# Optimization experiments

Measured on AMD Instinct MI355X. Metric: run time of the kernel, lower is better.

## Reference

```python
import jax, jax.numpy as jnp
import numpy as np
from jax import lax

NEG = -1e30  # log-space -inf surrogate

def setup_inputs() -> dict:
    key = jax.random.key(0)
    ks = jax.random.split(key, 6)
    B, T, D, V, Lmax = 16, 800, 512, 4000, 100
    hs_pad = jax.random.normal(ks[0], (B, T, D), dtype=jnp.float32)
    W = jax.random.normal(ks[1], (D, V), dtype=jnp.float32) * 0.02
    b = jnp.zeros((V,), dtype=jnp.float32)
    hlens = jax.random.randint(ks[2], (B,), 400, T + 1, dtype=jnp.int32)
    ys_pad = jax.random.randint(ks[3], (B, Lmax), 1, V, dtype=jnp.int32)
    ys_lens = jax.random.randint(ks[4], (B,), 50, Lmax + 1, dtype=jnp.int32)
    return {"hs_pad": hs_pad, "W": W, "b": b, "hlens": hlens,
            "ys_pad": ys_pad, "ys_lens": ys_lens}

def _ctc_loss(lp, ys_pad, hlens, ys_lens):
    # lp: [T, B, V] log-probs; blank = 0
    T, B, V = lp.shape
    Lmax = ys_pad.shape[1]
    S = 2 * Lmax + 1  # extended label length: blank-interleaved
    ext = jnp.zeros((B, S), dtype=ys_pad.dtype).at[:, 1::2].set(ys_pad)
    # skip transition s-2 -> s allowed when ext[s] != blank and ext[s] != ext[s-2]
    skip = jnp.concatenate(
        [jnp.zeros((B, 2), dtype=bool),
         (ext[:, 2:] != 0) & (ext[:, 2:] != ext[:, :-2])], axis=1)
    # per-frame emission log-probs for extended labels: [T, B, S]
    emit = jnp.take_along_axis(lp, jnp.broadcast_to(ext[None], (T, B, S)), axis=2)
    alpha0 = jnp.full((B, S), NEG, dtype=lp.dtype).at[:, :2].set(emit[0, :, :2])

    def step(alpha, inp):
        emit_t, active = inp  # [B, S], [B]
        s1 = jnp.pad(alpha[:, :-1], ((0, 0), (1, 0)), constant_values=NEG)
        s2 = jnp.pad(alpha[:, :-2], ((0, 0), (2, 0)), constant_values=NEG)
        s2 = jnp.where(skip, s2, NEG)
        new = jnp.logaddexp(jnp.logaddexp(alpha, s1), s2) + emit_t
        alpha = jnp.where(active[:, None], new, alpha)  # freeze past hlen
        return alpha, None

    active = jnp.arange(1, T)[:, None] < hlens[None, :]  # [T-1, B]
    alpha, _ = lax.scan(step, alpha0, (emit[1:], active))
    idx = (2 * ys_lens).astype(jnp.int32)  # last blank position
    a_last = jnp.take_along_axis(alpha, idx[:, None], axis=1)[:, 0]
    a_prev = jnp.take_along_axis(alpha, (idx - 1)[:, None], axis=1)[:, 0]
    loss = -jnp.logaddexp(a_last, a_prev)
    # zero_infinity=True
    return jnp.where(jnp.isfinite(loss) & (loss < 1e29), loss, 0.0)

def reference(hs_pad, W, b, hlens, ys_pad, ys_lens):
    # ctc_lo projection (dropout_rate=0.0) -> [T, B, V] -> log_softmax
    logits = jnp.einsum('btd,dv->btv', hs_pad, W) + b
    lp = jax.nn.log_softmax(logits, axis=-1).transpose(1, 0, 2)
    loss = _ctc_loss(lp, ys_pad, hlens, ys_lens)
    B = hs_pad.shape[0]
    return loss.sum() / B  # reduce=True: sum / batch size
```

## Files before the change

kernel.cpp:

```cpp
#include <hip/hip_runtime.h>
#include <hip/hip_bf16.h>
#include <math.h>

#define NEGV -1e30f
#define LN2F 0.6931471805599453f


typedef __attribute__((ext_vector_type(8))) short bf16x8;
typedef __attribute__((ext_vector_type(4))) float f32x4;

__device__ __forceinline__ short f2bf(float x) {
    __hip_bfloat16 h = __float2bfloat16(x);
    return __builtin_bit_cast(short, h);
}

__device__ __forceinline__ float shup1(float x) {
    return __builtin_bit_cast(float,
        __builtin_amdgcn_update_dpp(0, __builtin_bit_cast(int, x),
                                    0x138, 0xf, 0xf, true));
}

#define GLD_LDS(g, l) \
    __builtin_amdgcn_global_load_lds( \
        (const __attribute__((address_space(1))) void*)(g), \
        (__attribute__((address_space(3))) void*)(l), 16, 0, 0)

#define WAITV(n) do { \
    asm volatile("s_waitcnt vmcnt(" #n ")" ::: "memory"); \
    __builtin_amdgcn_sched_barrier(0); \
} while (0)

__global__ __launch_bounds__(256) void prep(
    const float* __restrict__ hs, const float* __restrict__ W,
    const float* __restrict__ bias, const int* __restrict__ ys,
    short* __restrict__ W2, short* __restrict__ A2,
    float* __restrict__ biasp, unsigned char* __restrict__ M,
    unsigned char* __restrict__ canon, float* __restrict__ lse_sum,
    float* __restrict__ out)
{
    __shared__ float tile[32][65];
    __shared__ unsigned char mapl[4096];
    const int bx = blockIdx.x, tid = threadIdx.x;

    if (bx < 1024) {
        const int n0 = (bx & 63) * 64;
        const int k0 = (bx >> 6) * 32;
        #pragma unroll
        for (int p = 0; p < 8; p++) {
            int idx = p * 256 + tid;
            int k = idx >> 6, n = idx & 63;
            int gn = n0 + n;
            tile[k][n] = (gn < 4000) ? W[(size_t)(k0 + k) * 4000 + gn] : 0.0f;
        }
        __syncthreads();
        const int nn = tid >> 6, lane = tid & 63;
        const int l16 = lane & 15, quad = lane >> 4;
        const int ct = n0 >> 7, wn = (n0 >> 6) & 1, it = k0 >> 5;
        size_t chunk = ((((size_t)ct * 16 + it) * 2 + wn) * 4 + nn) * 64 + lane;
        bf16x8 r;
        #pragma unroll
        for (int j = 0; j < 8; j++) r[j] = f2bf(tile[quad * 8 + j][nn * 16 + l16]);
        *(bf16x8*)(W2 + chunk * 8) = r;
    } else if (bx < 4224) {
        int g = (bx - 1024) * 256 + tid;
        int lane = g & 63, mi = (g >> 6) & 3, wm = (g >> 8) & 1;
        int it = (g >> 9) & 15, rb = g >> 13;
        int row = rb * 128 + wm * 64 + mi * 16 + (lane & 15);
        int k = it * 32 + (lane >> 4) * 8;
        const float* src = hs + (size_t)row * 512 + k;
        float4 u = *(const float4*)src;
        float4 v = *(const float4*)(src + 4);
        bf16x8 r;
        r[0] = f2bf(u.x); r[1] = f2bf(u.y); r[2] = f2bf(u.z); r[3] = f2bf(u.w);
        r[4] = f2bf(v.x); r[5] = f2bf(v.y); r[6] = f2bf(v.z); r[7] = f2bf(v.w);
        *(bf16x8*)(A2 + (size_t)g * 8) = r;
    } else if (bx < 4240) {
        const int b = bx - 4224;
        for (int i = tid; i < 1024; i += 256)
            ((unsigned int*)mapl)[i] = 0xFFFFFFFFu;
        __syncthreads();
        if (tid == 0) mapl[0] = 0;
        __syncthreads();
        if (tid < 100) mapl[ys[b * 100 + tid]] = (unsigned char)(tid + 1);
        __syncthreads();
        for (int i = tid; i < 1024; i += 256)
            ((unsigned int*)(M + (size_t)b * 4096))[i] = ((const unsigned int*)mapl)[i];
        if (tid < 128) {
            int colc = (tid >= 1 && tid <= 100) ? ys[b * 100 + tid - 1] : 0;
            canon[b * 128 + tid] = mapl[colc];
        }
    } else {
        for (int i = tid; i < 4096; i += 256)
            biasp[i] = (i < 4000) ? bias[i] : NEGV;
        for (int i = tid; i < 12800; i += 256)
            lse_sum[i] = 0.0f;
        if (tid == 0) out[0] = 0.0f;
    }
}

__global__ __launch_bounds__(512, 4) void lse_mfma(
    const short* __restrict__ A2,
    const short* __restrict__ W2,
    const float* __restrict__ biasp,
    const unsigned char* __restrict__ M,
    float* __restrict__ lse_sum,
    __hip_bfloat16* __restrict__ Praw)
{
    const unsigned int bid = blockIdx.x;
    const unsigned int xcd = bid & 7;
    const unsigned int s = bid >> 3;
    const unsigned int cp = s / 13;
    const unsigned int rl = s - cp * 13;
    const unsigned int rb = rl * 8 + xcd;
    if (rb >= 100) return;

    const int tid = threadIdx.x;
    const int w = tid >> 6, lane = tid & 63;
    const int quad = lane >> 4, l16 = lane & 15;
    const int wm = w >> 2;
    const int wc = w & 3;
    const int row0 = rb * 128;
    const int col0 = cp * 256;

    __shared__ __align__(16) short sbuf[3][12288];

    const short* gb[3];
    int lo[3];
    #pragma unroll
    for (int j = 0; j < 3; j++) {
        int sg = 3 * w + j;
        const short* cbase =
            (sg < 8)  ? (A2 + (size_t)rb * 65536)
          : (sg < 16) ? (W2 + (size_t)(2 * cp) * 65536)
                      : (W2 + (size_t)(2 * cp + 1) * 65536);
        gb[j] = cbase + (sg & 7) * 512 + lane * 8;
        lo[j] = sg * 512 + lane * 8;
    }

#define STAGE(s_, bi_) do { \
    GLD_LDS(gb[0] + (size_t)(s_) * 4096, &sbuf[bi_][lo[0]]); \
    GLD_LDS(gb[1] + (size_t)(s_) * 4096, &sbuf[bi_][lo[1]]); \
    GLD_LDS(gb[2] + (size_t)(s_) * 4096, &sbuf[bi_][lo[2]]); \
} while (0)

    f32x4 acc[4][4];
    #pragma unroll
    for (int mi = 0; mi < 4; mi++)
        #pragma unroll
        for (int ni = 0; ni < 4; ni++) acc[mi][ni] = (f32x4){0.f,0.f,0.f,0.f};

    STAGE(0, 0);
    STAGE(1, 1);
    WAITV(3);
    __builtin_amdgcn_s_barrier();
    __builtin_amdgcn_sched_barrier(0);

    const int boff = 4096 + (wc >> 1) * 4096 + (wc & 1) * 2048;

    #pragma unroll
    for (int it = 0; it < 16; ++it) {
        if (it + 2 < 16) STAGE(it + 2, (it + 2) % 3);

        const short* cb = &sbuf[it % 3][0];
        const short* ap = cb + wm * 2048 + lane * 8;
        const short* bp = cb + boff + lane * 8;
        bf16x8 af[4], bfr[4];
        #pragma unroll
        for (int mi = 0; mi < 4; mi++) af[mi]  = *(const bf16x8*)(ap + mi * 512);
        #pragma unroll
        for (int ni = 0; ni < 4; ni++) bfr[ni] = *(const bf16x8*)(bp + ni * 512);

        __builtin_amdgcn_s_setprio(1);
        #pragma unroll
        for (int mi = 0; mi < 4; mi++)
            #pragma unroll
            for (int ni = 0; ni < 4; ni++)
                acc[mi][ni] = __builtin_amdgcn_mfma_f32_16x16x32_bf16(
                    af[mi], bfr[ni], acc[mi][ni], 0, 0, 0);
        __builtin_amdgcn_s_setprio(0);

        if (it < 15) {
            if (it < 14) { WAITV(3); }
            else         { WAITV(0); }
            __builtin_amdgcn_s_barrier();
            __builtin_amdgcn_sched_barrier(0);
        }
    }
#undef STAGE
    __builtin_amdgcn_sched_barrier(0);

    const int b0i = row0 / 800;
    const int b1i = (b0i + 1 < 16) ? b0i + 1 : 15;
    const int bbound = (b0i + 1) * 800;
    float sv[16];
    #pragma unroll
    for (int i = 0; i < 16; i++) sv[i] = 0.0f;
    #pragma unroll
    for (int ni = 0; ni < 4; ni++) {
        int col = col0 + wc * 64 + ni * 16 + l16;
        float bj = biasp[col];
        unsigned char sl0 = M[(size_t)b0i * 4096 + col];
        unsigned char sl1 = M[(size_t)b1i * 4096 + col];
        #pragma unroll
        for (int mi = 0; mi < 4; mi++) {
            #pragma unroll
            for (int r = 0; r < 4; r++) {
                int row = row0 + wm * 64 + mi * 16 + quad * 4 + r;
                float v = acc[mi][ni][r] + bj;
                sv[mi * 4 + r] += __expf(v);
                unsigned char sl = (row < bbound) ? sl0 : sl1;
                if (sl != 255)
                    Praw[(size_t)row * 128 + sl] = __float2bfloat16(v);
            }
        }
    }
    #pragma unroll
    for (int off = 1; off < 16; off <<= 1)
        #pragma unroll
        for (int i = 0; i < 16; i++) sv[i] += __shfl_xor(sv[i], off);
    if (l16 == 0) {
        #pragma unroll
        for (int mi = 0; mi < 4; mi++)
            #pragma unroll
            for (int r = 0; r < 4; r++)
                atomicAdd(&lse_sum[row0 + wm * 64 + mi * 16 + quad * 4 + r],
                          sv[mi * 4 + r]);
    }
}

__global__ __launch_bounds__(256) void pexp(
    const __hip_bfloat16* __restrict__ Praw,
    const float* __restrict__ lse_sum,
    const unsigned char* __restrict__ canon,
    float* __restrict__ PE)
{
    __shared__ unsigned char st[224];
    __shared__ float scs[16];
    const int bp = blockIdx.x;
    const int b = bp / 50, rr = bp - b * 50;
    const int tid = threadIdx.x;
    const unsigned char* cb = canon + b * 128;
    if (tid < 224) {
        int idx = (tid + 1) >> 1;
        st[tid] = (tid & 1) ? cb[idx < 128 ? idx : 127] : (unsigned char)0;
    }
    const int row0 = b * 800 + rr * 16;
    if (tid < 16) scs[tid] = __builtin_amdgcn_rcpf(lse_sum[row0 + tid]) * 2048.0f;
    __syncthreads();
    for (int item = tid; item < 832; item += 256) {
        int i = item / 52, sg = item - i * 52;
        int row = row0 + i;
        const __hip_bfloat16* pr = Praw + (size_t)row * 128;
        float sc = scs[i];
        int s0 = sg * 4;
        float4 o;
        o.x = (s0 + 0 <= 200) ? __expf(__bfloat162float(pr[st[s0 + 0]])) * sc : 0.f;
        o.y = (s0 + 1 <= 200) ? __expf(__bfloat162float(pr[st[s0 + 1]])) * sc : 0.f;
        o.z = (s0 + 2 <= 200) ? __expf(__bfloat162float(pr[st[s0 + 2]])) * sc : 0.f;
        o.w = (s0 + 3 <= 200) ? __expf(__bfloat162float(pr[st[s0 + 3]])) * sc : 0.f;
        *(float4*)&PE[(size_t)row * 208 + s0] = o;
    }
}

__global__ __launch_bounds__(256) void ctc_dp(
    const float* __restrict__ PE,
    const int* __restrict__ hlens,
    const int* __restrict__ ys,
    const int* __restrict__ ylens,
    float* __restrict__ out)
{
    const int b = blockIdx.x, tid = threadIdx.x;
    const int w = tid >> 6, lane = tid & 63;
    __shared__ float emS[3][13376];
    __shared__ float sA[256];

    const float* Pb = PE + (size_t)b * 800 * 208;
    const int hl = hlens[b], L = ylens[b];
    const int t_stop = hl - 1;
    const int C = (t_stop + 63) >> 6;

    const int yb = b * 100;
    float kA = 0.f, kB = 0.f, kH = 0.f;
    if (lane >= 1 && 2 * lane <= 99)
        kA = (ys[yb + 2 * lane] != ys[yb + 2 * lane - 1]) ? 1.f : 0.f;
    if (2 * lane + 1 <= 99)
        kB = (ys[yb + 2 * lane + 1] != ys[yb + 2 * lane]) ? 1.f : 0.f;
    if (lane >= 1 && 2 * lane - 1 <= 99)
        kH = (ys[yb + 2 * lane - 1] != ys[yb + 2 * lane - 2]) ? 1.f : 0.f;
    const float m0  = (lane <= 50) ? 1.f : 0.f;
    const float m13 = (lane <= 49) ? 1.f : 0.f;

    float a0 = 0.f, a1 = 0.f, a2 = 0.f, a3 = 0.f;
    if (w == 0 && lane == 0) {
        a0 = Pb[0];
        a1 = Pb[1];
    }
    int kacc = 0;

#define STAGE_DP(nc_) do { \
    const char* _src = (const char*)(Pb + (size_t)(64 * (nc_) + 1) * 208); \
    char* _dst = (char*)&emS[(nc_) % 3][0]; \
    const int _base = tid - 64; \
    _Pragma("unroll") \
    for (int _j = 0; _j < 17; _j++) { \
        int _idx = _base + 192 * _j; \
        GLD_LDS(_src + (size_t)_idx * 16, _dst + (size_t)_idx * 16); \
    } \
    if (w == 1) { \
        int _idx = 3264 + lane; \
        GLD_LDS(_src + (size_t)_idx * 16, _dst + (size_t)_idx * 16); \
    } \
} while (0)

#define WAITCHUNK() do { \
    if (w == 1) { WAITV(18); } else { WAITV(17); } \
} while (0)

    if (w > 0) {
        STAGE_DP(0);
        STAGE_DP(1);
        WAITCHUNK();
    }
    __builtin_amdgcn_s_barrier();
    __builtin_amdgcn_sched_barrier(0);

    for (int ch = 0; ch < C; ch++) {
        if (w > 0) {
            if (ch + 2 < C) {
                STAGE_DP(ch + 2);
                WAITCHUNK();
            } else {
                WAITV(0);
            }
        } else {
            const float* bb = emS[ch % 3];
            const int t0 = 64 * ch + 1;
            const int soff = 4 * lane;
            if (t0 + 63 <= t_stop) {
                f32x4 e = *(const f32x4*)&bb[0 * 208 + soff];
                f32x4 f = *(const f32x4*)&bb[1 * 208 + soff];
                #pragma unroll
                for (int k = 0; k < 32; k++) {
                    f32x4 en = (f32x4){0.f,0.f,0.f,0.f};
                    f32x4 fn = (f32x4){0.f,0.f,0.f,0.f};
                    if (k < 31) {
                        en = *(const f32x4*)&bb[(2 * k + 2) * 208 + soff];
                        fn = *(const f32x4*)&bb[(2 * k + 3) * 208 + soff];
                    }
                    float pht = shup1(e[3]);
                    float h1 = shup1(a3);
                    float h2 = shup1(a2);
                    float h3 = shup1(a1);
                    float tm1 = fmaf(kH, h3, h1 + h2);
                    float t0v = a0 + h1;
                    float t1v = fmaf(kA, h1, a1 + a0);
                    float t2v = a2 + a1;
                    float t3v = fmaf(kB, a1, a3 + a2);
                    float um1 = pht * tm1;
                    float u0 = e[0] * t0v, u1 = e[1] * t1v;
                    float u2 = e[2] * t2v, u3 = e[3] * t3v;
                    a0 = (f[0] * (u0 + um1)) * m0;
                    a1 = (f[1] * fmaf(kA, um1, u1 + u0)) * m13;
                    a2 = (f[2] * (u2 + u1)) * m13;
                    a3 = (f[3] * fmaf(kB, u1, u3 + u2)) * m13;
                    if ((k & 7) == 7) {
                        int tc = t0 + 2 * k + 1;
                        float lm = fmaxf(fmaxf(a0, a1), fmaxf(a2, a3));
                        int sa1 = (2 * L < tc) ? 2 * L : tc;
                        int sa2 = (int)(2.0f * L * tc / hl);
                        float v1 = __shfl(lm, sa1 >> 2);
                        float v2 = __shfl(lm, sa2 >> 2);
                        float av = fmaxf(v1, v2);
                        int eb = (__float_as_int(av) >> 23) & 0xFF;
                        if (eb != 0 && eb != 255) {
                            int e2i = eb - 127;
                            kacc += e2i;
                            float sc = __int_as_float((127 - e2i) << 23);
                            a0 *= sc; a1 *= sc; a2 *= sc; a3 *= sc;
                        }
                    }
                    e = en; f = fn;
                }
            } else {
                for (int t = t0; t <= t_stop; t++) {
                    if ((t & 15) == 0) {
                        float lm = fmaxf(fmaxf(a0, a1), fmaxf(a2, a3));
                        int sa1 = (2 * L < t) ? 2 * L : t;
                        int sa2 = (int)(2.0f * L * t / hl);
                        float v1 = __shfl(lm, sa1 >> 2);
                        float v2 = __shfl(lm, sa2 >> 2);
                        float av = fmaxf(v1, v2);
                        int eb = (__float_as_int(av) >> 23) & 0xFF;
                        if (eb != 0 && eb != 255) {
                            int e2i = eb - 127;
                            kacc += e2i;
                            float sc = __int_as_float((127 - e2i) << 23);
                            a0 *= sc; a1 *= sc; a2 *= sc; a3 *= sc;
                        }
                    }
                    f32x4 e = *(const f32x4*)&bb[(t - t0) * 208 + soff];
                    float p3 = shup1(a3);
                    float n0 = (a0 + p3) * e[0];
                    float n1 = fmaf(kA, p3, a1 + a0) * e[1];
                    float n2 = (a2 + a1) * e[2];
                    float n3 = fmaf(kB, a1, a3 + a2) * e[3];
                    a0 = n0 * m0; a1 = n1 * m13; a2 = n2 * m13; a3 = n3 * m13;
                }
            }
        }
        __builtin_amdgcn_s_barrier();
        __builtin_amdgcn_sched_barrier(0);
    }
#undef STAGE_DP
#undef WAITCHUNK

    if (w == 0) {
        sA[lane * 4 + 0] = a0; sA[lane * 4 + 1] = a1;
        sA[lane * 4 + 2] = a2; sA[lane * 4 + 3] = a3;
    }
    __syncthreads();

    if (tid == 0) {
        int idx = 2 * L;
        float s = sA[idx] + sA[idx - 1];
        float la = __logf(s) + (float)(kacc - 11 * hl) * LN2F;
        float loss = -la;
        if (!isfinite(loss) || loss >= 1e29f) loss = 0.0f;
        atomicAdd(out, loss * 0.0625f);
    }
}

extern "C" void kernel_launch(void* const* d_in, const int* in_sizes, int n_in,
                              void* d_out, int out_size, void* d_ws, size_t ws_size,
                              hipStream_t stream)
{
    const float* hs    = (const float*)d_in[0];
    const float* W     = (const float*)d_in[1];
    const float* bias  = (const float*)d_in[2];
    const int*   hlens = (const int*)d_in[3];
    const int*   ys    = (const int*)d_in[4];
    const int*   ylens = (const int*)d_in[5];
    float* out = (float*)d_out;

    char* wsb = (char*)d_ws;
    short* W2      = (short*)(wsb);
    short* A2      = (short*)(wsb + 4194304);
    float* PE      = (float*)(wsb + 4194304);
    float* biasp   = (float*)(wsb + 17301504);
    __hip_bfloat16* Praw = (__hip_bfloat16*)(wsb + 17317888);
    float* lse_sum = (float*)(wsb + 20594688);
    unsigned char* M     = (unsigned char*)(wsb + 20645888);
    unsigned char* canon = (unsigned char*)(wsb + 20711424);

    hipLaunchKernelGGL(prep,     dim3(4241), dim3(256), 0, stream,
                       hs, W, bias, ys, W2, A2, biasp, M, canon, lse_sum, out);
    hipLaunchKernelGGL(lse_mfma, dim3(1664), dim3(512), 0, stream,
                       A2, W2, biasp, M, lse_sum, Praw);
    hipLaunchKernelGGL(pexp,     dim3(800),  dim3(256), 0, stream,
                       Praw, lse_sum, canon, PE);
    hipLaunchKernelGGL(ctc_dp,   dim3(16),   dim3(256), 0, stream,
                       PE, hlens, ys, ylens, out);
}
```

Baseline: 197.6 us.

## Load GEMM B operand directly into registers with double buffering, bypassing LDS

The W (B) tiles for the projection GEMM are now fetched with inline-asm global_load_dwordx4 straight into registers, alternating between two register buffers across iterations. Only the A tile still goes through the triple-buffered LDS pipeline, so shared memory per block shrinks from 3x12288 to 3x4096 shorts. The aim is to cut LDS traffic and footprint, which could also allow more resident blocks. The trade-off is more register pressure, duplicated global/L2 reads of B by waves that previously shared it through LDS, and correctness that depends on the hand-written vmcnt waits.

```diff
diff --git a/kernel.cpp b/kernel.cpp
--- a/kernel.cpp
+++ b/kernel.cpp
@@ -24,6 +24,10 @@
     __builtin_amdgcn_global_load_lds( \
         (const __attribute__((address_space(1))) void*)(g), \
         (__attribute__((address_space(3))) void*)(l), 16, 0, 0)
+
+#define LOADX4(dst, addr, off) \
+    asm volatile("global_load_dwordx4 %0, %1, off offset:" #off \
+                 : "=&v"(dst) : "v"(addr) : "memory")
 
 #define WAITV(n) do { \
     asm volatile("s_waitcnt vmcnt(" #n ")" ::: "memory"); \
@@ -122,25 +126,20 @@
     const int row0 = rb * 128;
     const int col0 = cp * 256;
 
-    __shared__ __align__(16) short sbuf[3][12288];
-
-    const short* gb[3];
-    int lo[3];
-    #pragma unroll
-    for (int j = 0; j < 3; j++) {
-        int sg = 3 * w + j;
-        const short* cbase =
-            (sg < 8)  ? (A2 + (size_t)rb * 65536)
-          : (sg < 16) ? (W2 + (size_t)(2 * cp) * 65536)
-                      : (W2 + (size_t)(2 * cp + 1) * 65536);
-        gb[j] = cbase + (sg & 7) * 512 + lane * 8;
-        lo[j] = sg * 512 + lane * 8;
-    }
-
-#define STAGE(s_, bi_) do { \
-    GLD_LDS(gb[0] + (size_t)(s_) * 4096, &sbuf[bi_][lo[0]]); \
-    GLD_LDS(gb[1] + (size_t)(s_) * 4096, &sbuf[bi_][lo[1]]); \
-    GLD_LDS(gb[2] + (size_t)(s_) * 4096, &sbuf[bi_][lo[2]]); \
+    __shared__ __align__(16) short sbuf[3][4096];
+
+    const short* gA = A2 + (size_t)rb * 65536 + w * 512 + lane * 8;
+    const int loA = w * 512 + lane * 8;
+
+#define STAGE(s_, bi_) GLD_LDS(gA + (size_t)(s_) * 4096, &sbuf[bi_][loA])
+
+    const short* Bgl = W2 + (size_t)(2 * cp + (wc >> 1)) * 65536
+                          + (wc & 1) * 2048 + lane * 8;
+
+#define LOADB(it_, bf_) do { \
+    const short* _b = Bgl + (size_t)(it_) * 4096; \
+    LOADX4(bf_[0], _b, 0);    LOADX4(bf_[1], _b, 1024); \
+    LOADX4(bf_[2], _b, 2048); LOADX4(bf_[3], _b, 3072); \
 } while (0)
 
     f32x4 acc[4][4];
@@ -149,44 +148,55 @@
         #pragma unroll
         for (int ni = 0; ni < 4; ni++) acc[mi][ni] = (f32x4){0.f,0.f,0.f,0.f};
 
+    bf16x8 bfA[4], bfB[4];
+
     STAGE(0, 0);
+    LOADB(0, bfA);
     STAGE(1, 1);
-    WAITV(3);
+    WAITV(1);
     __builtin_amdgcn_s_barrier();
     __builtin_amdgcn_sched_barrier(0);
 
-    const int boff = 4096 + (wc >> 1) * 4096 + (wc & 1) * 2048;
-
     #pragma unroll
     for (int it = 0; it < 16; ++it) {
+        if (it + 1 < 16) {
+            if ((it + 1) & 1) LOADB(it + 1, bfB);
+            else              LOADB(it + 1, bfA);
+        }
         if (it + 2 < 16) STAGE(it + 2, (it + 2) % 3);
 
-        const short* cb = &sbuf[it % 3][0];
-        const short* ap = cb + wm * 2048 + lane * 8;
-        const short* bp = cb + boff + lane * 8;
-        bf16x8 af[4], bfr[4];
-        #pragma unroll
-        for (int mi = 0; mi < 4; mi++) af[mi]  = *(const bf16x8*)(ap + mi * 512);
-        #pragma unroll
-        for (int ni = 0; ni < 4; ni++) bfr[ni] = *(const bf16x8*)(bp + ni * 512);
+        const short* ap = &sbuf[it % 3][wm * 2048 + lane * 8];
+        bf16x8 af[4];
+        #pragma unroll
+        for (int mi = 0; mi < 4; mi++) af[mi] = *(const bf16x8*)(ap + mi * 512);
 
         __builtin_amdgcn_s_setprio(1);
-        #pragma unroll
-        for (int mi = 0; mi < 4; mi++)
+        if (it & 1) {
             #pragma unroll
-            for (int ni = 0; ni < 4; ni++)
-                acc[mi][ni] = __builtin_amdgcn_mfma_f32_16x16x32_bf16(
-                    af[mi], bfr[ni], acc[mi][ni], 0, 0, 0);
+            for (int mi = 0; mi < 4; mi++)
+                #pragma unroll
+                for (int ni = 0; ni < 4; ni++)
+                    acc[mi][ni] = __builtin_amdgcn_mfma_f32_16x16x32_bf16(
+                        af[mi], bfB[ni], acc[mi][ni], 0, 0, 0);
+        } else {
+            #pragma unroll
+            for (int mi = 0; mi < 4; mi++)
+                #pragma unroll
+                for (int ni = 0; ni < 4; ni++)
+                    acc[mi][ni] = __builtin_amdgcn_mfma_f32_16x16x32_bf16(
+                        af[mi], bfA[ni], acc[mi][ni], 0, 0, 0);
+        }
         __builtin_amdgcn_s_setprio(0);
 
         if (it < 15) {
-            if (it < 14) { WAITV(3); }
+            if (it < 14) { WAITV(1); }
             else         { WAITV(0); }
             __builtin_amdgcn_s_barrier();
             __builtin_amdgcn_sched_barrier(0);
         }
     }
 #undef STAGE
+#undef LOADB
     __builtin_amdgcn_sched_barrier(0);
 
     const int b0i = row0 / 800;
```

Result: no change. 201.2 us (+1.8%).
